# Optimization experiments

Hardware: AMD Instinct MI355X
Metric: run time of the kernel (lower is better)

The kernel has to match this reference:

```python
import jax, jax.numpy as jnp
import numpy as np

N = 100_000      # nodes
E = 1_600_000    # edges
D_IN = 128       # input_dim
H = 128          # hidden_dim
L = 3            # num_layers
G = 128          # graphs in batch
EPS = 1e-5       # BatchNorm1d eps


def setup_inputs() -> dict:
    key = jax.random.key(0)
    ks = jax.random.split(key, 8)
    inp = {
        "x": jax.random.normal(ks[0], (N, D_IN), dtype=jnp.float32),
        "edge_index": jax.random.randint(ks[1], (2, E), 0, N),
        "batch": jnp.sort(jax.random.randint(ks[2], (N,), 0, G)),
    }
    for i in range(L):
        din = D_IN if i == 0 else H
        kw = jax.random.fold_in(key, 100 + i)
        inp[f"W{i}"] = jax.random.normal(kw, (din, H), dtype=jnp.float32) / np.sqrt(din).astype(np.float32)
        inp[f"b{i}"] = jnp.zeros((H,), jnp.float32)
        inp[f"g{i}"] = jnp.ones((H,), jnp.float32)
        inp[f"beta{i}"] = jnp.zeros((H,), jnp.float32)
    return inp


def _gcn_conv(x, W, b, src, dst, dinv):
    # GCNConv (normalize=True, add_self_loops=True):
    # out = D^{-1/2} (A + I) D^{-1/2} X W + b, deg computed on dst with self-loops
    h = x @ W                                   # [N,H]
    coef = (dinv[src] * dinv[dst])[:, None]     # per-edge norm
    agg = jax.ops.segment_sum(h[src] * coef, dst, num_segments=N)
    agg = agg + h * (dinv * dinv)[:, None]      # self-loop term deg^{-1}
    return agg + b


def _batchnorm(z, g, beta):
    mu = jnp.mean(z, axis=0)
    var = jnp.mean(jnp.square(z - mu), axis=0)  # biased var (training-mode BN)
    return (z - mu) * jax.lax.rsqrt(var + EPS) * g + beta


def reference(x, edge_index, batch,
              W0, b0, g0, beta0,
              W1, b1, g1, beta1,
              W2, b2, g2, beta2):
    src, dst = edge_index[0], edge_index[1]
    # degree of A + I on target index
    deg = jax.ops.segment_sum(jnp.ones((E,), x.dtype), dst, num_segments=N) + 1.0
    dinv = jax.lax.rsqrt(deg)
    params = [(W0, b0, g0, beta0), (W1, b1, g1, beta1), (W2, b2, g2, beta2)]
    zs = []
    h = x
    for (W, b, g, beta) in params:
        h = _gcn_conv(h, W, b, src, dst, dinv)
        h = jax.nn.relu(h)
        h = _batchnorm(h, g, beta)
        zs.append(h)
    pooled = [jax.ops.segment_sum(z, batch, num_segments=G) for z in zs]  # sum pool
    h_cat = jnp.concatenate(zs, axis=1)        # [N, L*H]
    g_cat = jnp.concatenate(pooled, axis=1)    # [G, L*H]
    return h_cat, g_cat
```

## Files before the change

kernel.cpp:

```cpp
#include <hip/hip_runtime.h>

#define NN 100000
#define NE 1600000
#define NG 128
#define BN_EPS 1e-5f
#define NBKT 64
#define AGG_BLOCKS 2048
#define AGG_WAVES (AGG_BLOCKS * 4)

typedef short s16x8 __attribute__((ext_vector_type(8)));
typedef float f32x4 __attribute__((ext_vector_type(4)));

static __device__ __forceinline__ unsigned short f2bf(float f) {
    unsigned u = __float_as_uint(f);
    u += 0x7fffu + ((u >> 16) & 1u);
    return (unsigned short)(u >> 16);
}
static __device__ __forceinline__ unsigned packbf(float a, float b) {
    return (unsigned)f2bf(a) | ((unsigned)f2bf(b) << 16);
}
static __device__ __forceinline__ float bf_lo(unsigned u) { return __uint_as_float(u << 16); }
static __device__ __forceinline__ float bf_hi(unsigned u) { return __uint_as_float(u & 0xffff0000u); }
static __device__ __forceinline__ float bf2f(ushort u) { return __uint_as_float((unsigned)u << 16); }

__global__ __launch_bounds__(256) void k_hist(const int* __restrict__ dst, int* __restrict__ deg) {
    int e = blockIdx.x * 256 + threadIdx.x;
    if (e < NE) atomicAdd(&deg[dst[e]], 1);
}

__global__ __launch_bounds__(256) void k_dinv(const int* __restrict__ deg, float* __restrict__ dinv) {
    int n = blockIdx.x * 256 + threadIdx.x;
    if (n < NN) dinv[n] = rsqrtf((float)deg[n] + 1.0f);
}

__global__ __launch_bounds__(256) void k_blockscan(const int* __restrict__ deg, int* __restrict__ excl,
                                                   int* __restrict__ bsum) {
    __shared__ int s[256];
    int t = threadIdx.x;
    int i = blockIdx.x * 256 + t;
    int v = (i < NN) ? deg[i] : 0;
    s[t] = v;
    __syncthreads();
    for (int o = 1; o < 256; o <<= 1) {
        int add = (t >= o) ? s[t - o] : 0;
        __syncthreads();
        s[t] += add;
        __syncthreads();
    }
    if (i < NN) excl[i] = s[t] - v;
    if (t == 255) bsum[blockIdx.x] = s[255];
}

__global__ __launch_bounds__(512) void k_scanb(int* __restrict__ bsum, int nb, int* __restrict__ row_start) {
    __shared__ int s[512];
    int t = threadIdx.x;
    int v = (t < nb) ? bsum[t] : 0;
    s[t] = v;
    __syncthreads();
    for (int o = 1; o < 512; o <<= 1) {
        int add = (t >= o) ? s[t - o] : 0;
        __syncthreads();
        s[t] += add;
        __syncthreads();
    }
    if (t < nb) bsum[t] = s[t] - v;
    if (t == nb - 1) row_start[NN] = s[t];
}

__global__ __launch_bounds__(256) void k_scanadd(int* __restrict__ row_start, const int* __restrict__ bsum) {
    int i = blockIdx.x * 256 + threadIdx.x;
    if (i < NN) row_start[i] += bsum[blockIdx.x];
}

__global__ __launch_bounds__(256) void k_fill(const int* __restrict__ src, const int* __restrict__ dst,
                                              const float* __restrict__ dinv, const int* __restrict__ row_start,
                                              int* __restrict__ cursor, int2* __restrict__ epair) {
    int e = blockIdx.x * 256 + threadIdx.x;
    if (e >= NE) return;
    int s = src[e], d = dst[e];
    float cf = dinv[s] * dinv[d];
    int pos = row_start[d] + atomicAdd(&cursor[d], 1);
    epair[pos] = make_int2(s, __float_as_int(cf));
}

__global__ __launch_bounds__(256) void k_cast(const float* __restrict__ x, uint4* __restrict__ xb) {
    int i = blockIdx.x * 256 + threadIdx.x;
    if (i >= NN * 16) return;
    float4 a = *(const float4*)(x + (size_t)i * 8);
    float4 b = *(const float4*)(x + (size_t)i * 8 + 4);
    uint4 o;
    o.x = packbf(a.x, a.y);
    o.y = packbf(a.z, a.w);
    o.z = packbf(b.x, b.y);
    o.w = packbf(b.z, b.w);
    xb[i] = o;
}

__global__ __launch_bounds__(64) void k_wfrag(const float* __restrict__ W, ushort* __restrict__ Wf) {
    int unit = blockIdx.x;
    int lane = threadIdx.x;
    int ks = unit >> 3, nb = unit & 7;
    int n = nb * 16 + (lane & 15);
    int k0 = ks * 32 + (lane >> 4) * 8;
    ushort o[8];
#pragma unroll
    for (int j = 0; j < 8; ++j) o[j] = f2bf(W[(size_t)(k0 + j) * 128 + n]);
    ushort* p = Wf + ((size_t)unit * 64 + lane) * 8;
#pragma unroll
    for (int j = 0; j < 8; ++j) p[j] = o[j];
}

__global__ __launch_bounds__(64) void k_wscale(const ushort* __restrict__ Wfb, const float* __restrict__ svec,
                                               ushort* __restrict__ Wff) {
    int unit = blockIdx.x;
    int lane = threadIdx.x;
    int k0 = (unit >> 3) * 32 + (lane >> 4) * 8;
    const ushort* p = Wfb + ((size_t)unit * 64 + lane) * 8;
    ushort* o = Wff + ((size_t)unit * 64 + lane) * 8;
#pragma unroll
    for (int j = 0; j < 8; ++j) o[j] = f2bf(bf2f(p[j]) * svec[k0 + j]);
}

__global__ __launch_bounds__(128) void k_finalize(const float* __restrict__ S, const float* __restrict__ Q,
                                                  const float* __restrict__ gam, const float* __restrict__ bet,
                                                  float* __restrict__ svec, float* __restrict__ tvec,
                                                  const float* __restrict__ Wnext, float* __restrict__ tW) {
    __shared__ float ts[128];
    int c = threadIdx.x;
    float s = 0.f, q = 0.f;
    for (int k = 0; k < NBKT; ++k) {
        s += S[k * 128 + c];
        q += Q[k * 128 + c];
    }
    float mean = s / (float)NN;
    float var = q / (float)NN - mean * mean;
    float rstd = rsqrtf(fmaxf(var, 0.f) + BN_EPS);
    float sc = gam[c] * rstd;
    float sh = bet[c] - mean * sc;
    svec[c] = sc;
    tvec[c] = sh;
    ts[c] = sh;
    __syncthreads();
    if (Wnext) {
        float acc = 0.f;
        for (int k = 0; k < 128; ++k) acc += ts[k] * Wnext[(size_t)k * 128 + c];
        tW[c] = acc;
    }
}

__global__ __launch_bounds__(256) void k_gemm(const ushort* __restrict__ Xb, const ushort* __restrict__ Wf,
                                              const float* __restrict__ tW, ushort* __restrict__ hm) {
    int tid = threadIdx.x;
    int wid = tid >> 6, lane = tid & 63;
    int r0 = blockIdx.x * 64 + wid * 16;
    int m = lane & 15, g = lane >> 4;
    int xrow = r0 + m;
    int xr = (xrow < NN) ? xrow : (NN - 1);
    const ushort* Xrow = Xb + (size_t)xr * 128 + g * 8;
    f32x4 acc[8];
#pragma unroll
    for (int nb = 0; nb < 8; ++nb) acc[nb] = (f32x4){0.f, 0.f, 0.f, 0.f};
#pragma unroll
    for (int ks = 0; ks < 4; ++ks) {
        s16x8 af = *(const s16x8*)(Xrow + ks * 32);
#pragma unroll
        for (int nb = 0; nb < 8; ++nb) {
            s16x8 wf = *(const s16x8*)(Wf + ((size_t)(ks * 8 + nb) * 64 + lane) * 8);
            acc[nb] = __builtin_amdgcn_mfma_f32_16x16x32_bf16(wf, af, acc[nb], 0, 0, 0);
        }
    }
    if (xrow < NN) {
        ushort* orow = hm + (size_t)xrow * 128 + g * 4;
        if (tW) {
#pragma unroll
            for (int nb = 0; nb < 8; ++nb) {
                float4 tw = *(const float4*)(tW + nb * 16 + g * 4);
                ushort4 o;
                o.x = f2bf(acc[nb][0] + tw.x);
                o.y = f2bf(acc[nb][1] + tw.y);
                o.z = f2bf(acc[nb][2] + tw.z);
                o.w = f2bf(acc[nb][3] + tw.w);
                *(ushort4*)(orow + nb * 16) = o;
            }
        } else {
#pragma unroll
            for (int nb = 0; nb < 8; ++nb) {
                ushort4 o;
                o.x = f2bf(acc[nb][0]);
                o.y = f2bf(acc[nb][1]);
                o.z = f2bf(acc[nb][2]);
                o.w = f2bf(acc[nb][3]);
                *(ushort4*)(orow + nb * 16) = o;
            }
        }
    }
}

__global__ __launch_bounds__(256) void k_agg(const uint* __restrict__ hm32, const int2* __restrict__ epair,
                                             const int* __restrict__ rs, const float* __restrict__ dinv,
                                             const float* __restrict__ bias, uint* __restrict__ act,
                                             float* __restrict__ bnsum, float* __restrict__ bnsq) {
    __shared__ float ls[128], lq[128];
    int tid = threadIdx.x;
    if (tid < 128) { ls[tid] = 0.f; lq[tid] = 0.f; }
    __syncthreads();
    int lane = tid & 63;
    int wgid = blockIdx.x * 4 + (tid >> 6);
    float2 b2 = *(const float2*)(bias + lane * 2);
    float s0 = 0.f, s1 = 0.f, q0 = 0.f, q1 = 0.f;

    for (int n = wgid; n < NN; n += AGG_WAVES) {
        float di = dinv[n];
        float sc = di * di;
        uint self = hm32[(size_t)n * 64 + lane];
        float a0 = sc * bf_lo(self);
        float a1 = sc * bf_hi(self);

        int i  = __builtin_amdgcn_readfirstlane(rs[n]);
        int i1 = __builtin_amdgcn_readfirstlane(rs[n + 1]);

        int2 epv = make_int2(0, 0);
        if (i < i1) {
            int o = min(min(lane, 15), i1 - i - 1);
            epv = epair[i + o];
        }
        while (i < i1) {
            int cnt = i1 - i;
            cnt = (cnt > 16) ? 16 : cnt;
            int2 cur = epv;
            int inext = i + cnt;
            if (inext < i1) {
                int o = min(min(lane, 15), i1 - inext - 1);
                epv = epair[inext + o];
            }
            uint g[16];
#pragma unroll
            for (int u = 0; u < 16; ++u) {
                int sidx = __builtin_amdgcn_readlane(cur.x, min(u, cnt - 1));
                g[u] = hm32[(size_t)sidx * 64 + lane];
            }
#pragma unroll
            for (int u = 0; u < 16; ++u) {
                float c = __int_as_float(__builtin_amdgcn_readlane(cur.y, min(u, cnt - 1)));
                c = (u < cnt) ? c : 0.f;
                a0 += c * bf_lo(g[u]);
                a1 += c * bf_hi(g[u]);
            }
            i = inext;
        }
        float z0 = fmaxf(a0 + b2.x, 0.f);
        float z1 = fmaxf(a1 + b2.y, 0.f);
        act[(size_t)n * 64 + lane] = packbf(z0, z1);
        s0 += z0; s1 += z1;
        q0 += z0 * z0; q1 += z1 * z1;
    }
    atomicAdd(&ls[lane * 2],     s0);
    atomicAdd(&ls[lane * 2 + 1], s1);
    atomicAdd(&lq[lane * 2],     q0);
    atomicAdd(&lq[lane * 2 + 1], q1);
    __syncthreads();
    if (tid < 128) {
        int bkt = blockIdx.x & (NBKT - 1);
        atomicAdd(&bnsum[bkt * 128 + tid], ls[tid]);
        atomicAdd(&bnsq[bkt * 128 + tid],  lq[tid]);
    }
}

__global__ __launch_bounds__(128) void k_norm(const ushort* __restrict__ act, const float* __restrict__ svec,
                                              const float* __restrict__ tvec, const int* __restrict__ batch,
                                              float* __restrict__ out, float* __restrict__ gout, int lofs) {
    int c = threadIdx.x;
    int n0 = blockIdx.x * 64;
    if (n0 >= NN) return;
    int n1 = n0 + 64; if (n1 > NN) n1 = NN;
    float scale = svec[c];
    float shift = tvec[c];
    int cur = batch[n0];
    float acc = 0.f;
    for (int n = n0; n < n1; ++n) {
        float z = bf2f(act[(size_t)n * 128 + c]) * scale + shift;
        out[(size_t)n * 384 + lofs + c] = z;
        int bn = batch[n];
        if (bn != cur) {
            atomicAdd(&gout[(size_t)cur * 384 + lofs + c], acc);
            acc = 0.f;
            cur = bn;
        }
        acc += z;
    }
    atomicAdd(&gout[(size_t)cur * 384 + lofs + c], acc);
}

extern "C" void kernel_launch(void* const* d_in, const int* in_sizes, int n_in,
                              void* d_out, int out_size, void* d_ws, size_t ws_size,
                              hipStream_t stream) {
    const float* x = (const float*)d_in[0];
    const int* ei = (const int*)d_in[1];
    const int* src = ei;
    const int* dst = ei + NE;
    const int* batch = (const int*)d_in[2];
    const float *W[3], *b[3], *g[3], *beta[3];
    for (int l = 0; l < 3; ++l) {
        W[l]    = (const float*)d_in[3 + 4 * l];
        b[l]    = (const float*)d_in[4 + 4 * l];
        g[l]    = (const float*)d_in[5 + 4 * l];
        beta[l] = (const float*)d_in[6 + 4 * l];
    }
    float* out = (float*)d_out;
    float* gout = out + (size_t)NN * 384;

    char* ws = (char*)d_ws;
    size_t off = 0;
    auto alloc = [&](size_t bytes) -> char* {
        off = (off + 255) & ~(size_t)255;
        char* p = ws + off;
        off += bytes;
        return p;
    };
    ushort* xb       = (ushort*)alloc((size_t)NN * 256);
    ushort* act      = (ushort*)alloc((size_t)NN * 256);
    ushort* hm       = (ushort*)alloc((size_t)NN * 256);
    int2*   epair    = (int2*)alloc((size_t)NE * 8);
    int*    deg      = (int*)alloc((size_t)NN * 4);
    int*    cursor   = (int*)alloc((size_t)NN * 4);
    int*    row_start= (int*)alloc((size_t)(NN + 1) * 4);
    float*  dinv     = (float*)alloc((size_t)NN * 4);
    int*    bsum     = (int*)alloc(512 * 4);
    float*  bnst     = (float*)alloc((size_t)3 * 2 * NBKT * 128 * 4);
    ushort* Wf       = (ushort*)alloc(3 * 16384 * 2);
    ushort* Wff      = (ushort*)alloc(16384 * 2);
    float*  svt      = (float*)alloc(3 * 2 * 128 * 4);
    float*  tW       = (float*)alloc(128 * 4);
    (void)ws_size;

    hipMemsetAsync(deg, 0, (size_t)NN * 4, stream);
    hipMemsetAsync(cursor, 0, (size_t)NN * 4, stream);
    hipMemsetAsync(bnst, 0, (size_t)3 * 2 * NBKT * 128 * 4, stream);
    hipMemsetAsync(gout, 0, (size_t)NG * 384 * 4, stream);

    int nbN = (NN + 255) / 256;
    int nbE = (NE + 255) / 256;

    k_hist<<<nbE, 256, 0, stream>>>(dst, deg);
    k_dinv<<<nbN, 256, 0, stream>>>(deg, dinv);
    k_blockscan<<<nbN, 256, 0, stream>>>(deg, row_start, bsum);
    k_scanb<<<1, 512, 0, stream>>>(bsum, nbN, row_start);
    k_scanadd<<<nbN, 256, 0, stream>>>(row_start, bsum);
    k_fill<<<nbE, 256, 0, stream>>>(src, dst, dinv, row_start, cursor, epair);
    k_cast<<<(NN * 16 + 255) / 256, 256, 0, stream>>>(x, (uint4*)xb);
    for (int l = 0; l < 3; ++l) k_wfrag<<<32, 64, 0, stream>>>(W[l], Wf + l * 16384);

    for (int l = 0; l < 3; ++l) {
        float* S = bnst + (size_t)l * 2 * NBKT * 128;
        float* Q = S + NBKT * 128;
        float* sv = svt + l * 256;
        float* tv = sv + 128;
        const ushort* gin = (l == 0) ? xb : act;
        const ushort* wfrag = (l == 0) ? (Wf + 0) : Wff;
        const float* tw_in = (l == 0) ? nullptr : tW;

        k_gemm<<<(NN + 63) / 64, 256, 0, stream>>>(gin, wfrag, tw_in, hm);
        k_agg<<<AGG_BLOCKS, 256, 0, stream>>>((const uint*)hm, epair, row_start, dinv, b[l],
                                              (uint*)act, S, Q);
        k_finalize<<<1, 128, 0, stream>>>(S, Q, g[l], beta[l], sv, tv,
                                          (l < 2) ? W[l + 1] : nullptr, tW);
        if (l < 2) k_wscale<<<32, 64, 0, stream>>>(Wf + (l + 1) * 16384, sv, Wff);
        k_norm<<<(NN + 63) / 64, 128, 0, stream>>>(act, sv, tv, batch, out, gout, l * 128);
    }
}
```

Before: 556.7 us.

## Build CSR via two-level bucket sort and fold dinv into GEMM output

Replaces the per-node atomic histogram, three-kernel scan and atomic scatter fill with a coarse 1024-node bucket sort: a bucket histogram, a bucket scan, a binning pass into a temp array, and a per-bucket kernel that builds row_start, dinv and the sorted source list in shared memory. The symmetric normalization is refactored so the GEMM scales each row by dinv[src] and aggregation multiplies the summed neighbors by dinv[dst]. The edge list shrinks from int2 (src, coef) to int, which halves index traffic in each aggregation pass. Padding lanes read a zeroed dummy row in place of a coefficient mask. The cost is an extra temp buffer and pass, and bucket partitioning that assumes NN fits in 128 buckets of 1024 nodes.

```diff
diff --git a/kernel.cpp b/kernel.cpp
--- a/kernel.cpp
+++ b/kernel.cpp
@@ -7,6 +7,9 @@
 #define NBKT 64
 #define AGG_BLOCKS 2048
 #define AGG_WAVES (AGG_BLOCKS * 4)
+#define NBUCK 98
+#define BIN_BLOCKS 256
+#define BIN_CHUNK 6250
 
 typedef short s16x8 __attribute__((ext_vector_type(8)));
 typedef float f32x4 __attribute__((ext_vector_type(4)));
@@ -23,64 +26,100 @@
 static __device__ __forceinline__ float bf_hi(unsigned u) { return __uint_as_float(u & 0xffff0000u); }
 static __device__ __forceinline__ float bf2f(ushort u) { return __uint_as_float((unsigned)u << 16); }
 
-__global__ __launch_bounds__(256) void k_hist(const int* __restrict__ dst, int* __restrict__ deg) {
-    int e = blockIdx.x * 256 + threadIdx.x;
-    if (e < NE) atomicAdd(&deg[dst[e]], 1);
-}
-
-__global__ __launch_bounds__(256) void k_dinv(const int* __restrict__ deg, float* __restrict__ dinv) {
-    int n = blockIdx.x * 256 + threadIdx.x;
-    if (n < NN) dinv[n] = rsqrtf((float)deg[n] + 1.0f);
-}
-
-__global__ __launch_bounds__(256) void k_blockscan(const int* __restrict__ deg, int* __restrict__ excl,
-                                                   int* __restrict__ bsum) {
-    __shared__ int s[256];
+__global__ __launch_bounds__(256) void k_bhist(const int* __restrict__ dst, int* __restrict__ gbh) {
+    __shared__ int lh[128];
     int t = threadIdx.x;
-    int i = blockIdx.x * 256 + t;
-    int v = (i < NN) ? deg[i] : 0;
+    if (t < 128) lh[t] = 0;
+    __syncthreads();
+    for (int e = blockIdx.x * 256 + t; e < NE; e += gridDim.x * 256)
+        atomicAdd(&lh[dst[e] >> 10], 1);
+    __syncthreads();
+    if (t < 128 && lh[t]) atomicAdd(&gbh[t], lh[t]);
+}
+
+__global__ __launch_bounds__(128) void k_bscan(const int* __restrict__ gbh, int* __restrict__ gbase,
+                                               int* __restrict__ gcur, int* __restrict__ row_start) {
+    __shared__ int s[128];
+    int t = threadIdx.x;
+    int v = gbh[t];
     s[t] = v;
     __syncthreads();
+    for (int o = 1; o < 128; o <<= 1) {
+        int a = (t >= o) ? s[t - o] : 0;
+        __syncthreads();
+        s[t] += a;
+        __syncthreads();
+    }
+    int ex = s[t] - v;
+    gbase[t] = ex;
+    gcur[t] = ex;
+    if (t == 127) { gbase[128] = s[127]; row_start[NN] = NE; }
+}
+
+__global__ __launch_bounds__(256) void k_bin(const int* __restrict__ src, const int* __restrict__ dst,
+                                             int* __restrict__ gcur, int* __restrict__ tmp) {
+    __shared__ int lh[128], lb[128], lc[128];
+    int t = threadIdx.x;
+    if (t < 128) lh[t] = 0;
+    __syncthreads();
+    int e0 = blockIdx.x * BIN_CHUNK, e1 = e0 + BIN_CHUNK;
+    for (int e = e0 + t; e < e1; e += 256) atomicAdd(&lh[dst[e] >> 10], 1);
+    __syncthreads();
+    if (t < 128) {
+        int c = lh[t];
+        lb[t] = c ? atomicAdd(&gcur[t], c) : 0;
+        lc[t] = 0;
+    }
+    __syncthreads();
+    for (int e = e0 + t; e < e1; e += 256) {
+        int d = dst[e];
+        int b = d >> 10;
+        int off = atomicAdd(&lc[b], 1);
+        tmp[lb[b] + off] = (src[e] << 10) | (d & 1023);
+    }
+}
+
+__global__ __launch_bounds__(256) void k_csr(const int* __restrict__ tmp, const int* __restrict__ gbase,
+                                             int* __restrict__ esrc, int* __restrict__ row_start,
+                                             float* __restrict__ dinv) {
+    __shared__ int h[1024], hs[1024], part[256];
+    int b = blockIdx.x, t = threadIdx.x;
+    int base = gbase[b], end = gbase[b + 1];
+#pragma unroll
+    for (int k = 0; k < 4; ++k) h[t * 4 + k] = 0;
+    __syncthreads();
+    for (int i = base + t; i < end; i += 256) atomicAdd(&h[tmp[i] & 1023], 1);
+    __syncthreads();
+    int l0 = h[t * 4], l1 = h[t * 4 + 1], l2 = h[t * 4 + 2], l3 = h[t * 4 + 3];
+    int ssum = l0 + l1 + l2 + l3;
+    part[t] = ssum;
+    __syncthreads();
     for (int o = 1; o < 256; o <<= 1) {
-        int add = (t >= o) ? s[t - o] : 0;
+        int a = (t >= o) ? part[t - o] : 0;
         __syncthreads();
-        s[t] += add;
+        part[t] += a;
         __syncthreads();
     }
-    if (i < NN) excl[i] = s[t] - v;
-    if (t == 255) bsum[blockIdx.x] = s[255];
-}
-
-__global__ __launch_bounds__(512) void k_scanb(int* __restrict__ bsum, int nb, int* __restrict__ row_start) {
-    __shared__ int s[512];
-    int t = threadIdx.x;
-    int v = (t < nb) ? bsum[t] : 0;
-    s[t] = v;
-    __syncthreads();
-    for (int o = 1; o < 512; o <<= 1) {
-        int add = (t >= o) ? s[t - o] : 0;
-        __syncthreads();
-        s[t] += add;
-        __syncthreads();
-    }
-    if (t < nb) bsum[t] = s[t] - v;
-    if (t == nb - 1) row_start[NN] = s[t];
-}
-
-__global__ __launch_bounds__(256) void k_scanadd(int* __restrict__ row_start, const int* __restrict__ bsum) {
-    int i = blockIdx.x * 256 + threadIdx.x;
-    if (i < NN) row_start[i] += bsum[blockIdx.x];
-}
-
-__global__ __launch_bounds__(256) void k_fill(const int* __restrict__ src, const int* __restrict__ dst,
-                                              const float* __restrict__ dinv, const int* __restrict__ row_start,
-                                              int* __restrict__ cursor, int2* __restrict__ epair) {
-    int e = blockIdx.x * 256 + threadIdx.x;
-    if (e >= NE) return;
-    int s = src[e], d = dst[e];
-    float cf = dinv[s] * dinv[d];
-    int pos = row_start[d] + atomicAdd(&cursor[d], 1);
-    epair[pos] = make_int2(s, __float_as_int(cf));
+    int ex = part[t] - ssum;
+    hs[t * 4]     = ex;
+    hs[t * 4 + 1] = ex + l0;
+    hs[t * 4 + 2] = ex + l0 + l1;
+    hs[t * 4 + 3] = ex + l0 + l1 + l2;
+    int n0 = b * 1024 + t * 4;
+#pragma unroll
+    for (int k = 0; k < 4; ++k) {
+        int n = n0 + k;
+        if (n < NN) {
+            row_start[n] = base + hs[t * 4 + k];
+            dinv[n] = rsqrtf((float)h[t * 4 + k] + 1.0f);
+        }
+    }
+    __syncthreads();
+    for (int i = base + t; i < end; i += 256) {
+        int rec = tmp[i];
+        int pos = atomicAdd(&hs[rec & 1023], 1);
+        esrc[base + pos] = rec >> 10;
+    }
 }
 
 __global__ __launch_bounds__(256) void k_cast(const float* __restrict__ x, uint4* __restrict__ xb) {
@@ -149,7 +188,8 @@
 }
 
 __global__ __launch_bounds__(256) void k_gemm(const ushort* __restrict__ Xb, const ushort* __restrict__ Wf,
-                                              const float* __restrict__ tW, ushort* __restrict__ hm) {
+                                              const float* __restrict__ tW, const float* __restrict__ dinv,
+                                              ushort* __restrict__ hm) {
     int tid = threadIdx.x;
     int wid = tid >> 6, lane = tid & 63;
     int r0 = blockIdx.x * 64 + wid * 16;
@@ -170,33 +210,34 @@
         }
     }
     if (xrow < NN) {
+        float ds = dinv[xr];
         ushort* orow = hm + (size_t)xrow * 128 + g * 4;
         if (tW) {
 #pragma unroll
             for (int nb = 0; nb < 8; ++nb) {
                 float4 tw = *(const float4*)(tW + nb * 16 + g * 4);
                 ushort4 o;
-                o.x = f2bf(acc[nb][0] + tw.x);
-                o.y = f2bf(acc[nb][1] + tw.y);
-                o.z = f2bf(acc[nb][2] + tw.z);
-                o.w = f2bf(acc[nb][3] + tw.w);
+                o.x = f2bf(ds * (acc[nb][0] + tw.x));
+                o.y = f2bf(ds * (acc[nb][1] + tw.y));
+                o.z = f2bf(ds * (acc[nb][2] + tw.z));
+                o.w = f2bf(ds * (acc[nb][3] + tw.w));
                 *(ushort4*)(orow + nb * 16) = o;
             }
         } else {
 #pragma unroll
             for (int nb = 0; nb < 8; ++nb) {
                 ushort4 o;
-                o.x = f2bf(acc[nb][0]);
-                o.y = f2bf(acc[nb][1]);
-                o.z = f2bf(acc[nb][2]);
-                o.w = f2bf(acc[nb][3]);
+                o.x = f2bf(ds * acc[nb][0]);
+                o.y = f2bf(ds * acc[nb][1]);
+                o.z = f2bf(ds * acc[nb][2]);
+                o.w = f2bf(ds * acc[nb][3]);
                 *(ushort4*)(orow + nb * 16) = o;
             }
         }
     }
 }
 
-__global__ __launch_bounds__(256) void k_agg(const uint* __restrict__ hm32, const int2* __restrict__ epair,
+__global__ __launch_bounds__(256) void k_agg(const uint* __restrict__ hm32, const int* __restrict__ esrc,
                                              const int* __restrict__ rs, const float* __restrict__ dinv,
                                              const float* __restrict__ bias, uint* __restrict__ act,
                                              float* __restrict__ bnsum, float* __restrict__ bnsq) {
@@ -210,46 +251,40 @@
     float s0 = 0.f, s1 = 0.f, q0 = 0.f, q1 = 0.f;
 
     for (int n = wgid; n < NN; n += AGG_WAVES) {
-        float di = dinv[n];
-        float sc = di * di;
         uint self = hm32[(size_t)n * 64 + lane];
-        float a0 = sc * bf_lo(self);
-        float a1 = sc * bf_hi(self);
+        float a0 = bf_lo(self);
+        float a1 = bf_hi(self);
 
         int i  = __builtin_amdgcn_readfirstlane(rs[n]);
         int i1 = __builtin_amdgcn_readfirstlane(rs[n + 1]);
 
-        int2 epv = make_int2(0, 0);
-        if (i < i1) {
-            int o = min(min(lane, 15), i1 - i - 1);
-            epv = epair[i + o];
-        }
+        int idxv = 0;
+        if (i < i1) idxv = esrc[i + min(min(lane, 15), i1 - i - 1)];
+
         while (i < i1) {
             int cnt = i1 - i;
             cnt = (cnt > 16) ? 16 : cnt;
-            int2 cur = epv;
+            int cur = idxv;
             int inext = i + cnt;
-            if (inext < i1) {
-                int o = min(min(lane, 15), i1 - inext - 1);
-                epv = epair[inext + o];
-            }
+            if (inext < i1)
+                idxv = esrc[inext + min(min(lane, 15), i1 - inext - 1)];
             uint g[16];
 #pragma unroll
             for (int u = 0; u < 16; ++u) {
-                int sidx = __builtin_amdgcn_readlane(cur.x, min(u, cnt - 1));
+                int sidx = __builtin_amdgcn_readlane(cur, u);
+                sidx = (u < cnt) ? sidx : NN;
                 g[u] = hm32[(size_t)sidx * 64 + lane];
             }
 #pragma unroll
             for (int u = 0; u < 16; ++u) {
-                float c = __int_as_float(__builtin_amdgcn_readlane(cur.y, min(u, cnt - 1)));
-                c = (u < cnt) ? c : 0.f;
-                a0 += c * bf_lo(g[u]);
-                a1 += c * bf_hi(g[u]);
+                a0 += bf_lo(g[u]);
+                a1 += bf_hi(g[u]);
             }
             i = inext;
         }
-        float z0 = fmaxf(a0 + b2.x, 0.f);
-        float z1 = fmaxf(a1 + b2.y, 0.f);
+        float di = dinv[n];
+        float z0 = fmaxf(fmaf(di, a0, b2.x), 0.f);
+        float z1 = fmaxf(fmaf(di, a1, b2.y), 0.f);
         act[(size_t)n * 64 + lane] = packbf(z0, z1);
         s0 += z0; s1 += z1;
         q0 += z0 * z0; q1 += z1 * z1;
@@ -319,34 +354,31 @@
     };
     ushort* xb       = (ushort*)alloc((size_t)NN * 256);
     ushort* act      = (ushort*)alloc((size_t)NN * 256);
-    ushort* hm       = (ushort*)alloc((size_t)NN * 256);
-    int2*   epair    = (int2*)alloc((size_t)NE * 8);
-    int*    deg      = (int*)alloc((size_t)NN * 4);
-    int*    cursor   = (int*)alloc((size_t)NN * 4);
+    ushort* hm       = (ushort*)alloc((size_t)(NN + 1) * 256);
+    int*    esrc     = (int*)alloc((size_t)NE * 4);
+    int*    tmp      = (int*)alloc((size_t)NE * 4);
     int*    row_start= (int*)alloc((size_t)(NN + 1) * 4);
     float*  dinv     = (float*)alloc((size_t)NN * 4);
-    int*    bsum     = (int*)alloc(512 * 4);
     float*  bnst     = (float*)alloc((size_t)3 * 2 * NBKT * 128 * 4);
     ushort* Wf       = (ushort*)alloc(3 * 16384 * 2);
     ushort* Wff      = (ushort*)alloc(16384 * 2);
     float*  svt      = (float*)alloc(3 * 2 * 128 * 4);
     float*  tW       = (float*)alloc(128 * 4);
+    int*    misc     = (int*)alloc(512 * 4);
+    int* gbh   = misc;
+    int* gbase = misc + 128;
+    int* gcur  = misc + 384;
     (void)ws_size;
 
-    hipMemsetAsync(deg, 0, (size_t)NN * 4, stream);
-    hipMemsetAsync(cursor, 0, (size_t)NN * 4, stream);
+    hipMemsetAsync(gbh, 0, 128 * 4, stream);
+    hipMemsetAsync(hm + (size_t)NN * 128, 0, 256, stream);
     hipMemsetAsync(bnst, 0, (size_t)3 * 2 * NBKT * 128 * 4, stream);
     hipMemsetAsync(gout, 0, (size_t)NG * 384 * 4, stream);
 
-    int nbN = (NN + 255) / 256;
-    int nbE = (NE + 255) / 256;
-
-    k_hist<<<nbE, 256, 0, stream>>>(dst, deg);
-    k_dinv<<<nbN, 256, 0, stream>>>(deg, dinv);
-    k_blockscan<<<nbN, 256, 0, stream>>>(deg, row_start, bsum);
-    k_scanb<<<1, 512, 0, stream>>>(bsum, nbN, row_start);
-    k_scanadd<<<nbN, 256, 0, stream>>>(row_start, bsum);
-    k_fill<<<nbE, 256, 0, stream>>>(src, dst, dinv, row_start, cursor, epair);
+    k_bhist<<<512, 256, 0, stream>>>(dst, gbh);
+    k_bscan<<<1, 128, 0, stream>>>(gbh, gbase, gcur, row_start);
+    k_bin<<<BIN_BLOCKS, 256, 0, stream>>>(src, dst, gcur, tmp);
+    k_csr<<<NBUCK, 256, 0, stream>>>(tmp, gbase, esrc, row_start, dinv);
     k_cast<<<(NN * 16 + 255) / 256, 256, 0, stream>>>(x, (uint4*)xb);
     for (int l = 0; l < 3; ++l) k_wfrag<<<32, 64, 0, stream>>>(W[l], Wf + l * 16384);
 
@@ -359,8 +391,8 @@
         const ushort* wfrag = (l == 0) ? (Wf + 0) : Wff;
         const float* tw_in = (l == 0) ? nullptr : tW;
 
-        k_gemm<<<(NN + 63) / 64, 256, 0, stream>>>(gin, wfrag, tw_in, hm);
-        k_agg<<<AGG_BLOCKS, 256, 0, stream>>>((const uint*)hm, epair, row_start, dinv, b[l],
+        k_gemm<<<(NN + 63) / 64, 256, 0, stream>>>(gin, wfrag, tw_in, dinv, hm);
+        k_agg<<<AGG_BLOCKS, 256, 0, stream>>>((const uint*)hm, esrc, row_start, dinv, b[l],
                                               (uint*)act, S, Q);
         k_finalize<<<1, 128, 0, stream>>>(S, Q, g[l], beta[l], sv, tv,
                                           (l < 2) ? W[l + 1] : nullptr, tW);
```

Result: faster. 473.1 us (-15.0%).
